# Optimization experiments

Hardware: AMD Instinct MI355X
Metric: run time of the kernel (lower is better)

Reference implementation:

```python
import jax, jax.numpy as jnp
import numpy as np

B, S, D_IN, D_H = 8, 4096, 256, 512
EPS = 1e-6


def setup_inputs() -> dict:
    key = jax.random.key(0)
    ks = jax.random.split(key, 5)
    scale = 1.0 / np.sqrt(D_IN)  # torch Linear default init scale (uniform bound)
    x = jax.random.normal(ks[0], (B, S, D_IN), dtype=jnp.float32)
    Wi = jax.random.normal(ks[1], (D_IN, D_H), dtype=jnp.float32) * scale
    Wf = jax.random.normal(ks[2], (D_IN, D_H), dtype=jnp.float32) * scale
    Wo = jax.random.normal(ks[3], (D_IN, D_H), dtype=jnp.float32) * scale
    Wz = jax.random.normal(ks[4], (D_IN, D_H), dtype=jnp.float32) * scale
    zb = jnp.zeros((D_H,), dtype=jnp.float32)
    return {"x": x, "Wi": Wi, "bi": zb, "Wf": Wf, "bf": zb,
            "Wo": Wo, "bo": zb, "Wz": Wz, "bz": zb}


def _xlstm_forward(x, Wi, bi, Wf, bf, Wo, bo, Wz, bz):
    # Batched projections over all timesteps at once: [B,S,D_H] each.
    i_t = jnp.exp(jnp.clip(jnp.einsum('bsd,dh->bsh', x, Wi) + bi, -20.0, 0.0))
    f_t = jnp.exp(jnp.clip(jnp.einsum('bsd,dh->bsh', x, Wf) + bf, -20.0, 0.0))
    o_t = jax.nn.sigmoid(jnp.einsum('bsd,dh->bsh', x, Wo) + bo)
    z_t = jnp.tanh(jnp.einsum('bsd,dh->bsh', x, Wz) + bz)

    def step(carry, gates):
        c, n = carry
        i, f, o, z = gates
        c = f * c + i * z
        n = f * n + i
        h = o * (c / (n + EPS))
        return (c, n), h

    c0 = jnp.zeros((x.shape[0], Wi.shape[1]), dtype=x.dtype)
    n0 = jnp.ones((x.shape[0], Wi.shape[1]), dtype=x.dtype)
    # time-major scan over the recurrence
    gates_tm = tuple(jnp.swapaxes(g, 0, 1) for g in (i_t, f_t, o_t, z_t))  # [S,B,H]
    _, h_tm = jax.lax.scan(step, (c0, n0), gates_tm)
    return jnp.swapaxes(h_tm, 0, 1)  # [B,S,H]


def reference(x, Wi, bi, Wf, bf, Wo, bo, Wz, bz):
    return _xlstm_forward(x, Wi, bi, Wf, bf, Wo, bo, Wz, bz)
```

## Files before the change

kernel.cpp:

```cpp
#include <hip/hip_runtime.h>
#include <hip/hip_bf16.h>
#include <cstdint>
#include <cstddef>

typedef __hip_bfloat16 bf16;
typedef __attribute__((ext_vector_type(8))) short short8;
typedef __attribute__((ext_vector_type(4))) short short4v;
typedef __attribute__((ext_vector_type(4))) float floatx4;

#define BB 8
#define SS 4096
#define DIN 256
#define DH 512
#define NCH 256
#define CHUNK 16

__device__ __forceinline__ float b2f(bf16 v) { return __bfloat162float(v); }
__device__ __forceinline__ float sh2f(short v) {
    unsigned int u = ((unsigned int)(unsigned short)v) << 16;
    float f; __builtin_memcpy(&f, &u, 4); return f;
}
__device__ __forceinline__ float frcp(float x) { return __builtin_amdgcn_rcpf(x); }
__device__ __forceinline__ short f2sh(float a) {
    bf16 bv = __float2bfloat16(a);
    short sv; __builtin_memcpy(&sv, &bv, 2); return sv;
}

__global__ __launch_bounds__(256) void convert_x(
    const float* __restrict__ X, bf16* __restrict__ Xb)
{
    const int idx = blockIdx.x * 256 + threadIdx.x;
    float4 v = ((const float4*)X)[idx];
    bf16 o[4] = {__float2bfloat16(v.x), __float2bfloat16(v.y),
                 __float2bfloat16(v.z), __float2bfloat16(v.w)};
    ((short4v*)Xb)[idx] = *(const short4v*)o;
}

__global__ __launch_bounds__(256) void transpose_w(
    const float* __restrict__ Wi, const float* __restrict__ Wf,
    const float* __restrict__ Wo, const float* __restrict__ Wz,
    bf16* __restrict__ Wt)
{
    int o = blockIdx.x * 256 + threadIdx.x;
    int r = o >> 8;
    int k = o & 255;
    int y = r >> 7;
    int c = r & 127;
    int g = c >> 5;
    int h = y * 32 + (c & 31);
    const float* W = (g == 0) ? Wi : (g == 1) ? Wf : (g == 2) ? Wo : Wz;
    Wt[o] = __float2bfloat16(W[(size_t)k * DH + h]);
}

__device__ __forceinline__ void load16_lds(const bf16* g, short* l)
{
    __builtin_amdgcn_global_load_lds(
        (const __attribute__((address_space(1))) unsigned int*)g,
        (__attribute__((address_space(3))) unsigned int*)l,
        16, 0, 0);
}

__global__ __launch_bounds__(256) void gemm_mfma(
    const bf16* __restrict__ Xb, const bf16* __restrict__ Wt,
    const float* __restrict__ bi, const float* __restrict__ bfv,
    const float* __restrict__ bo, const float* __restrict__ bz,
    bf16* __restrict__ Pi, bf16* __restrict__ Pf,
    bf16* __restrict__ Po, bf16* __restrict__ Pz,
    float* __restrict__ Aa, float* __restrict__ Bca, float* __restrict__ Bna,
    int nb)
{
    __shared__ __align__(16) short smem[3 * 8192];

    const int cpx = gridDim.x >> 3;
    const int logical = ((int)blockIdx.x & 7) * cpx + ((int)blockIdx.x >> 3);
    const int y  = logical & 15;
    const int m0 = (logical >> 4) * 128;
    const int n0 = y * 128;

    const int tid  = threadIdx.x;
    const int wave = tid >> 6, lane = tid & 63;
    const int wm   = (wave >> 1) * 64, wn = (wave & 1) * 64;
    const int l15  = lane & 15;
    const int q    = lane >> 4;

    floatx4 acc[4][4];
#pragma unroll
    for (int i = 0; i < 4; i++)
#pragma unroll
        for (int j = 0; j < 4; j++) acc[i][j] = (floatx4){0.f, 0.f, 0.f, 0.f};

    const int r_ld = tid >> 2;
    const int c_ld = tid & 3;
    const bf16* agp0 = Xb + (size_t)(m0 + r_ld) * DIN + c_ld * 8;
    const bf16* agp1 = Xb + (size_t)(m0 + 64 + r_ld) * DIN + c_ld * 8;
    const bf16* bgp0 = Wt + (size_t)(n0 + r_ld) * DIN + c_ld * 8;
    const bf16* bgp1 = Wt + (size_t)(n0 + 64 + r_ld) * DIN + c_ld * 8;

#define STAGE(K0, BUF)                                            \
    do {                                                          \
        short* A_ = smem + (BUF) * 8192;                          \
        short* B_ = A_ + 4096;                                    \
        load16_lds(agp0 + (K0), &A_[tid * 8]);                    \
        load16_lds(agp1 + (K0), &A_[2048 + tid * 8]);             \
        load16_lds(bgp0 + (K0), &B_[tid * 8]);                    \
        load16_lds(bgp1 + (K0), &B_[2048 + tid * 8]);             \
    } while (0)

    STAGE(0, 0);
    STAGE(32, 1);

#pragma unroll
    for (int k = 0; k < 8; k++) {
        if (k < 6) STAGE((k + 2) * 32, (k + 2) % 3);
        if (k < 6)       asm volatile("s_waitcnt vmcnt(8)" ::: "memory");
        else if (k == 6) asm volatile("s_waitcnt vmcnt(4)" ::: "memory");
        else             asm volatile("s_waitcnt vmcnt(0)" ::: "memory");
        __builtin_amdgcn_s_barrier();
        __builtin_amdgcn_sched_barrier(0);

        const short* A = smem + (k % 3) * 8192;
        const short* B = A + 4096;
        short8 af[4], bfr[4];
#pragma unroll
        for (int ti = 0; ti < 4; ti++)
            af[ti] = *(const short8*)&A[(wm + ti * 16 + l15) * 32 + q * 8];
#pragma unroll
        for (int tj = 0; tj < 4; tj++)
            bfr[tj] = *(const short8*)&B[(wn + tj * 16 + l15) * 32 + q * 8];
#pragma unroll
        for (int ti = 0; ti < 4; ti++)
#pragma unroll
            for (int tj = 0; tj < 4; tj++)
                acc[ti][tj] = __builtin_amdgcn_mfma_f32_16x16x32_bf16(
                    af[ti], bfr[tj], acc[ti][tj], 0, 0, 0);
        asm volatile("s_waitcnt lgkmcnt(0)" ::: "memory");
        __builtin_amdgcn_sched_barrier(0);
        __builtin_amdgcn_s_barrier();
    }
#undef STAGE

#pragma unroll
    for (int ti = 0; ti < 4; ti++) {
        const int mrow = wm + ti * 16 + q * 4;
#pragma unroll
        for (int tj = 0; tj < 4; tj++) {
            const int cb = wn + tj * 16;
            const int g  = cb >> 5;
            const int c  = cb + l15;
            const float* bp = (g == 0) ? bi : (g == 1) ? bfv
                            : (g == 2) ? bo : bz;
            const float bsv = bp[y * 32 + (c & 31)];
#pragma unroll
            for (int r = 0; r < 4; r++) {
                const float v = acc[ti][tj][r] + bsv;
                float a;
                if (g == 0 || g == 1) {
                    a = __expf(fminf(fmaxf(v, -20.f), 0.f));
                } else if (g == 2) {
                    a = frcp(1.f + __expf(-v));
                } else {
                    a = 1.f - 2.f * frcp(__expf(2.f * v) + 1.f);
                }
                smem[(mrow + r) * 132 + c] = f2sh(a);
            }
        }
    }
    __syncthreads();

    const int bidx = m0 / SS;

    {
        const int cp  = (tid & 31) * 4;
        const int g2  = cp >> 5;
        const int hb  = y * 32 + (cp & 31);
        bf16* pl = ((g2 == 0) ? Pi : (g2 == 1) ? Pf : (g2 == 2) ? Po : Pz) + hb;
        const int r0 = tid >> 5;
#pragma unroll
        for (int t = 0; t < 16; t++) {
            const int row = t * 8 + r0;
            short4v v = *(const short4v*)&smem[row * 132 + cp];
            *(short4v*)(pl + (size_t)(m0 + row) * DH) = v;
        }
    }

    {
        const int hh = tid & 31;
        const int ch = tid >> 5;
        float A = 1.f, Bc = 0.f, Bn = 0.f;
        const short* base = &smem[(ch * CHUNK) * 132];
#pragma unroll
        for (int s = 0; s < CHUNK; s++) {
            const short* rp = base + s * 132;
            const float iv = sh2f(rp[hh]);
            const float f  = sh2f(rp[32 + hh]);
            const float zv = sh2f(rp[96 + hh]);
            Bc = fmaf(f, Bc, iv * zv);
            Bn = fmaf(f, Bn, iv);
            A *= f;
        }
        const int ch_g = ((m0 % SS) >> 4) + ch;
        const int hgl  = y * 32 + hh;
        const size_t cidx = (size_t)(ch_g * nb + bidx) * DH + hgl;
        Aa[cidx] = A; Bca[cidx] = Bc; Bna[cidx] = Bn;
    }
}

__global__ __launch_bounds__(256) void scan_chunks(
    float* __restrict__ Aa, float* __restrict__ Bca,
    const float* __restrict__ Bna, int nb)
{
    __shared__ float sA[4][64], sBc[4][64], sBn[4][64];
    const int tid = threadIdx.x;
    const int t   = blockIdx.x * 64 + (tid & 63);
    const int s   = tid >> 6;
    const int stride = nb * DH;
    const int SEG = NCH / 4;

    float A = 1.f, Bc = 0.f, Bn = 0.f;
    for (int k = 0; k < SEG; k++) {
        const size_t cidx = (size_t)(s * SEG + k) * stride + t;
        const float a  = Aa[cidx];
        const float bc = Bca[cidx];
        const float bn = Bna[cidx];
        Bc = fmaf(a, Bc, bc);
        Bn = fmaf(a, Bn, bn);
        A *= a;
    }
    sA[s][tid & 63] = A; sBc[s][tid & 63] = Bc; sBn[s][tid & 63] = Bn;
    __syncthreads();

    float c = 0.f, n = 1.f;
#pragma unroll
    for (int s2 = 0; s2 < 3; s2++) {
        if (s2 < s) {
            const float a  = sA[s2][tid & 63];
            const float nc = fmaf(a, c, sBc[s2][tid & 63]);
            n = fmaf(a, n, sBn[s2][tid & 63]);
            c = nc;
        }
    }

    for (int k = 0; k < SEG; k++) {
        const size_t cidx = (size_t)(s * SEG + k) * stride + t;
        const float a  = Aa[cidx];
        const float bc = Bca[cidx];
        const float bn = Bna[cidx];
        Aa[cidx] = c; Bca[cidx] = n;
        const float nc = fmaf(a, c, bc);
        n = fmaf(a, n, bn);
        c = nc;
    }
}

__global__ __launch_bounds__(256) void scan_emit(
    const bf16* __restrict__ Pi, const bf16* __restrict__ Pf,
    const bf16* __restrict__ Po, const bf16* __restrict__ Pz,
    const float* __restrict__ Cs, const float* __restrict__ Ns,
    float* __restrict__ out, int nb)
{
    const int tid = threadIdx.x;
    const int ch  = blockIdx.x * 2 + (tid >> 7);
    const int b   = blockIdx.y;
    const int hg  = (tid & 127) * 4;
    const size_t base = ((size_t)(b * SS + ch * CHUNK)) * DH + hg;
    const size_t cidx = (size_t)(ch * nb + b) * DH + hg;

    float c[4], n[4];
    *(floatx4*)c = *(const floatx4*)(Cs + cidx);
    *(floatx4*)n = *(const floatx4*)(Ns + cidx);

#pragma unroll 4
    for (int s = 0; s < CHUNK; s++) {
        const size_t o = base + (size_t)s * DH;
        short4v i4 = *(const short4v*)(Pi + o);
        short4v f4 = *(const short4v*)(Pf + o);
        short4v o4 = *(const short4v*)(Po + o);
        short4v z4 = *(const short4v*)(Pz + o);
        float h[4];
#pragma unroll
        for (int j = 0; j < 4; j++) {
            const float f  = sh2f(f4[j]);
            const float iv = sh2f(i4[j]);
            const float ov = sh2f(o4[j]);
            const float zv = sh2f(z4[j]);
            c[j] = fmaf(f, c[j], iv * zv);
            n[j] = fmaf(f, n[j], iv);
            h[j] = ov * c[j] * frcp(n[j] + 1e-6f);
        }
        *(floatx4*)(out + o) = *(floatx4*)h;
    }
}

extern "C" void kernel_launch(void* const* d_in, const int* in_sizes, int n_in,
                              void* d_out, int out_size, void* d_ws, size_t ws_size,
                              hipStream_t stream)
{
    const float* x   = (const float*)d_in[0];
    const float* Wi  = (const float*)d_in[1];
    const float* bi  = (const float*)d_in[2];
    const float* Wf  = (const float*)d_in[3];
    const float* bfv = (const float*)d_in[4];
    const float* Wo  = (const float*)d_in[5];
    const float* bo  = (const float*)d_in[6];
    const float* Wz  = (const float*)d_in[7];
    const float* bz  = (const float*)d_in[8];
    float* out = (float*)d_out;

    int nb = BB;
    while (nb > 1) {
        size_t need = (1u << 20)
                    + (size_t)nb * SS * DIN * 2
                    + 4 * (size_t)nb * SS * DH * 2
                    + 3 * (size_t)NCH * nb * DH * 4;
        if (need <= ws_size) break;
        nb >>= 1;
    }

    const size_t plane = (size_t)nb * SS * DH;
    bf16* Wt = (bf16*)d_ws;
    bf16* Xb = (bf16*)((char*)d_ws + (1u << 20));
    bf16* Pi = Xb + (size_t)nb * SS * DIN;
    bf16* Pf = Pi + plane;
    bf16* Po = Pf + plane;
    bf16* Pz = Po + plane;
    float* Aa  = (float*)(Pz + plane);
    float* Bca = Aa  + (size_t)NCH * nb * DH;
    float* Bna = Bca + (size_t)NCH * nb * DH;

    transpose_w<<<2048, 256, 0, stream>>>(Wi, Wf, Wo, Wz, Wt);

    for (int b0 = 0; b0 < BB; b0 += nb) {
        const float* Xsrc = x   + (size_t)b0 * SS * DIN;
        float*       Ob   = out + (size_t)b0 * SS * DH;
        convert_x<<<nb * 1024, 256, 0, stream>>>(Xsrc, Xb);
        gemm_mfma<<<nb * 512, 256, 0, stream>>>(
            Xb, Wt, bi, bfv, bo, bz, Pi, Pf, Po, Pz, Aa, Bca, Bna, nb);
        scan_chunks<<<nb * 8, 256, 0, stream>>>(Aa, Bca, Bna, nb);
        scan_emit<<<dim3(NCH / 2, nb), 256, 0, stream>>>(
            Pi, Pf, Po, Pz, Aa, Bca, Ob, nb);
    }
}
```

Before: 233.2 us.

## Recompute gate GEMM in emit pass instead of storing bf16 gate planes

Drops the four bf16 gate planes written by the GEMM and read back by scan_emit. The GEMM is now a template that runs twice: the first pass produces only per-chunk scan summaries, and the second pass recomputes the gates and emits h directly from the chunk carries. This trades roughly 64 MB of intermediate traffic for a second GEMM. It also shrinks shared memory and swaps the 3-stage load pipeline for a simpler 2-stage loop that waits on vmcnt(0) every iteration, which may expose more load latency.

```diff
diff --git a/kernel.cpp b/kernel.cpp
--- a/kernel.cpp
+++ b/kernel.cpp
@@ -15,7 +15,6 @@
 #define NCH 256
 #define CHUNK 16
 
-__device__ __forceinline__ float b2f(bf16 v) { return __bfloat162float(v); }
 __device__ __forceinline__ float sh2f(short v) {
     unsigned int u = ((unsigned int)(unsigned short)v) << 16;
     float f; __builtin_memcpy(&f, &u, 4); return f;
@@ -60,16 +59,15 @@
         16, 0, 0);
 }
 
-__global__ __launch_bounds__(256) void gemm_mfma(
+template<int MODE>
+__global__ __launch_bounds__(256) void gemm_fused(
     const bf16* __restrict__ Xb, const bf16* __restrict__ Wt,
     const float* __restrict__ bi, const float* __restrict__ bfv,
     const float* __restrict__ bo, const float* __restrict__ bz,
-    bf16* __restrict__ Pi, bf16* __restrict__ Pf,
-    bf16* __restrict__ Po, bf16* __restrict__ Pz,
     float* __restrict__ Aa, float* __restrict__ Bca, float* __restrict__ Bna,
-    int nb)
-{
-    __shared__ __align__(16) short smem[3 * 8192];
+    float* __restrict__ out, int nb)
+{
+    __shared__ __align__(16) short smem[128 * 132];
 
     const int cpx = gridDim.x >> 3;
     const int logical = ((int)blockIdx.x & 7) * cpx + ((int)blockIdx.x >> 3);
@@ -107,18 +105,14 @@
     } while (0)
 
     STAGE(0, 0);
-    STAGE(32, 1);
+    asm volatile("s_waitcnt vmcnt(0)" ::: "memory");
+    __builtin_amdgcn_s_barrier();
 
 #pragma unroll
     for (int k = 0; k < 8; k++) {
-        if (k < 6) STAGE((k + 2) * 32, (k + 2) % 3);
-        if (k < 6)       asm volatile("s_waitcnt vmcnt(8)" ::: "memory");
-        else if (k == 6) asm volatile("s_waitcnt vmcnt(4)" ::: "memory");
-        else             asm volatile("s_waitcnt vmcnt(0)" ::: "memory");
-        __builtin_amdgcn_s_barrier();
-        __builtin_amdgcn_sched_barrier(0);
-
-        const short* A = smem + (k % 3) * 8192;
+        const int cur = k & 1;
+        if (k < 7) STAGE((k + 1) * 32, cur ^ 1);
+        const short* A = smem + cur * 8192;
         const short* B = A + 4096;
         short8 af[4], bfr[4];
 #pragma unroll
@@ -133,8 +127,7 @@
             for (int tj = 0; tj < 4; tj++)
                 acc[ti][tj] = __builtin_amdgcn_mfma_f32_16x16x32_bf16(
                     af[ti], bfr[tj], acc[ti][tj], 0, 0, 0);
-        asm volatile("s_waitcnt lgkmcnt(0)" ::: "memory");
-        __builtin_amdgcn_sched_barrier(0);
+        asm volatile("s_waitcnt vmcnt(0) lgkmcnt(0)" ::: "memory");
         __builtin_amdgcn_s_barrier();
     }
 #undef STAGE
@@ -146,6 +139,7 @@
         for (int tj = 0; tj < 4; tj++) {
             const int cb = wn + tj * 16;
             const int g  = cb >> 5;
+            if (MODE == 0 && g == 2) continue;
             const int c  = cb + l15;
             const float* bp = (g == 0) ? bi : (g == 1) ? bfv
                             : (g == 2) ? bo : bz;
@@ -168,26 +162,14 @@
     __syncthreads();
 
     const int bidx = m0 / SS;
-
-    {
-        const int cp  = (tid & 31) * 4;
-        const int g2  = cp >> 5;
-        const int hb  = y * 32 + (cp & 31);
-        bf16* pl = ((g2 == 0) ? Pi : (g2 == 1) ? Pf : (g2 == 2) ? Po : Pz) + hb;
-        const int r0 = tid >> 5;
-#pragma unroll
-        for (int t = 0; t < 16; t++) {
-            const int row = t * 8 + r0;
-            short4v v = *(const short4v*)&smem[row * 132 + cp];
-            *(short4v*)(pl + (size_t)(m0 + row) * DH) = v;
-        }
-    }
-
-    {
-        const int hh = tid & 31;
-        const int ch = tid >> 5;
+    const int hh   = tid & 31;
+    const int ch   = tid >> 5;
+    const int ch_g = ((m0 % SS) >> 4) + ch;
+    const size_t cidx = (size_t)(ch_g * nb + bidx) * DH + y * 32 + hh;
+    const short* base = &smem[(ch * CHUNK) * 132];
+
+    if (MODE == 0) {
         float A = 1.f, Bc = 0.f, Bn = 0.f;
-        const short* base = &smem[(ch * CHUNK) * 132];
 #pragma unroll
         for (int s = 0; s < CHUNK; s++) {
             const short* rp = base + s * 132;
@@ -198,10 +180,22 @@
             Bn = fmaf(f, Bn, iv);
             A *= f;
         }
-        const int ch_g = ((m0 % SS) >> 4) + ch;
-        const int hgl  = y * 32 + hh;
-        const size_t cidx = (size_t)(ch_g * nb + bidx) * DH + hgl;
         Aa[cidx] = A; Bca[cidx] = Bc; Bna[cidx] = Bn;
+    } else {
+        float c = Aa[cidx];
+        float n = Bca[cidx];
+        float* orow = out + (size_t)(m0 + ch * CHUNK) * DH + y * 32 + hh;
+#pragma unroll
+        for (int s = 0; s < CHUNK; s++) {
+            const short* rp = base + s * 132;
+            const float iv = sh2f(rp[hh]);
+            const float f  = sh2f(rp[32 + hh]);
+            const float ov = sh2f(rp[64 + hh]);
+            const float zv = sh2f(rp[96 + hh]);
+            c = fmaf(f, c, iv * zv);
+            n = fmaf(f, n, iv);
+            orow[(size_t)s * DH] = ov * c * frcp(n + 1e-6f);
+        }
     }
 }
 
@@ -249,45 +243,6 @@
         const float nc = fmaf(a, c, bc);
         n = fmaf(a, n, bn);
         c = nc;
-    }
-}
-
-__global__ __launch_bounds__(256) void scan_emit(
-    const bf16* __restrict__ Pi, const bf16* __restrict__ Pf,
-    const bf16* __restrict__ Po, const bf16* __restrict__ Pz,
-    const float* __restrict__ Cs, const float* __restrict__ Ns,
-    float* __restrict__ out, int nb)
-{
-    const int tid = threadIdx.x;
-    const int ch  = blockIdx.x * 2 + (tid >> 7);
-    const int b   = blockIdx.y;
-    const int hg  = (tid & 127) * 4;
-    const size_t base = ((size_t)(b * SS + ch * CHUNK)) * DH + hg;
-    const size_t cidx = (size_t)(ch * nb + b) * DH + hg;
-
-    float c[4], n[4];
-    *(floatx4*)c = *(const floatx4*)(Cs + cidx);
-    *(floatx4*)n = *(const floatx4*)(Ns + cidx);
-
-#pragma unroll 4
-    for (int s = 0; s < CHUNK; s++) {
-        const size_t o = base + (size_t)s * DH;
-        short4v i4 = *(const short4v*)(Pi + o);
-        short4v f4 = *(const short4v*)(Pf + o);
-        short4v o4 = *(const short4v*)(Po + o);
-        short4v z4 = *(const short4v*)(Pz + o);
-        float h[4];
-#pragma unroll
-        for (int j = 0; j < 4; j++) {
-            const float f  = sh2f(f4[j]);
-            const float iv = sh2f(i4[j]);
-            const float ov = sh2f(o4[j]);
-            const float zv = sh2f(z4[j]);
-            c[j] = fmaf(f, c[j], iv * zv);
-            n[j] = fmaf(f, n[j], iv);
-            h[j] = ov * c[j] * frcp(n[j] + 1e-6f);
-        }
-        *(floatx4*)(out + o) = *(floatx4*)h;
     }
 }
 
@@ -310,20 +265,14 @@
     while (nb > 1) {
         size_t need = (1u << 20)
                     + (size_t)nb * SS * DIN * 2
-                    + 4 * (size_t)nb * SS * DH * 2
                     + 3 * (size_t)NCH * nb * DH * 4;
         if (need <= ws_size) break;
         nb >>= 1;
     }
 
-    const size_t plane = (size_t)nb * SS * DH;
     bf16* Wt = (bf16*)d_ws;
     bf16* Xb = (bf16*)((char*)d_ws + (1u << 20));
-    bf16* Pi = Xb + (size_t)nb * SS * DIN;
-    bf16* Pf = Pi + plane;
-    bf16* Po = Pf + plane;
-    bf16* Pz = Po + plane;
-    float* Aa  = (float*)(Pz + plane);
+    float* Aa  = (float*)(Xb + (size_t)nb * SS * DIN);
     float* Bca = Aa  + (size_t)NCH * nb * DH;
     float* Bna = Bca + (size_t)NCH * nb * DH;
 
@@ -333,10 +282,10 @@
         const float* Xsrc = x   + (size_t)b0 * SS * DIN;
         float*       Ob   = out + (size_t)b0 * SS * DH;
         convert_x<<<nb * 1024, 256, 0, stream>>>(Xsrc, Xb);
-        gemm_mfma<<<nb * 512, 256, 0, stream>>>(
-            Xb, Wt, bi, bfv, bo, bz, Pi, Pf, Po, Pz, Aa, Bca, Bna, nb);
+        gemm_fused<0><<<nb * 512, 256, 0, stream>>>(
+            Xb, Wt, bi, bfv, bo, bz, Aa, Bca, Bna, nullptr, nb);
         scan_chunks<<<nb * 8, 256, 0, stream>>>(Aa, Bca, Bna, nb);
-        scan_emit<<<dim3(NCH / 2, nb), 256, 0, stream>>>(
-            Pi, Pf, Po, Pz, Aa, Bca, Ob, nb);
-    }
-}
+        gemm_fused<1><<<nb * 512, 256, 0, stream>>>(
+            Xb, Wt, bi, bfv, bo, bz, Aa, Bca, Bna, Ob, nb);
+    }
+}
```

Result: slower. 241.8 us (+3.7%).

## Merge weight transpose and x conversion into one prep kernel; double-buffer GEMM

Applied to the files above, without the earlier changes.

Combines the weight transpose/bf16 cast and the x-to-bf16 conversion into a single prep launch, which saves one kernel launch per call. The GEMM goes from a three-stage to a two-stage LDS pipeline and drops the sched_barrier hints. The LDS array is resized to 128*132 shorts, which still covers the two 8192-short buffers and leaves room that the unseen epilogue may use for staging. Less prefetch depth may expose more global-load latency, but the lower LDS use could allow more resident blocks.

```diff
diff --git a/kernel.cpp b/kernel.cpp
--- a/kernel.cpp
+++ b/kernel.cpp
@@ -15,7 +15,6 @@
 #define NCH 256
 #define CHUNK 16
 
-__device__ __forceinline__ float b2f(bf16 v) { return __bfloat162float(v); }
 __device__ __forceinline__ float sh2f(short v) {
     unsigned int u = ((unsigned int)(unsigned short)v) << 16;
     float f; __builtin_memcpy(&f, &u, 4); return f;
@@ -26,30 +25,31 @@
     short sv; __builtin_memcpy(&sv, &bv, 2); return sv;
 }
 
-__global__ __launch_bounds__(256) void convert_x(
-    const float* __restrict__ X, bf16* __restrict__ Xb)
-{
-    const int idx = blockIdx.x * 256 + threadIdx.x;
-    float4 v = ((const float4*)X)[idx];
-    bf16 o[4] = {__float2bfloat16(v.x), __float2bfloat16(v.y),
-                 __float2bfloat16(v.z), __float2bfloat16(v.w)};
-    ((short4v*)Xb)[idx] = *(const short4v*)o;
-}
-
-__global__ __launch_bounds__(256) void transpose_w(
+__global__ __launch_bounds__(256) void prep(
     const float* __restrict__ Wi, const float* __restrict__ Wf,
     const float* __restrict__ Wo, const float* __restrict__ Wz,
-    bf16* __restrict__ Wt)
-{
-    int o = blockIdx.x * 256 + threadIdx.x;
-    int r = o >> 8;
-    int k = o & 255;
-    int y = r >> 7;
-    int c = r & 127;
-    int g = c >> 5;
-    int h = y * 32 + (c & 31);
-    const float* W = (g == 0) ? Wi : (g == 1) ? Wf : (g == 2) ? Wo : Wz;
-    Wt[o] = __float2bfloat16(W[(size_t)k * DH + h]);
+    bf16* __restrict__ Wt,
+    const float* __restrict__ X, bf16* __restrict__ Xb, int tblk)
+{
+    const int bx = blockIdx.x;
+    const int tid = threadIdx.x;
+    if (bx < tblk) {
+        int o = bx * 256 + tid;
+        int r = o >> 8;
+        int k = o & 255;
+        int y = r >> 7;
+        int c = r & 127;
+        int g = c >> 5;
+        int h = y * 32 + (c & 31);
+        const float* W = (g == 0) ? Wi : (g == 1) ? Wf : (g == 2) ? Wo : Wz;
+        Wt[o] = __float2bfloat16(W[(size_t)k * DH + h]);
+    } else {
+        const int idx = (bx - tblk) * 256 + tid;
+        float4 v = ((const float4*)X)[idx];
+        bf16 o4[4] = {__float2bfloat16(v.x), __float2bfloat16(v.y),
+                      __float2bfloat16(v.z), __float2bfloat16(v.w)};
+        ((short4v*)Xb)[idx] = *(const short4v*)o4;
+    }
 }
 
 __device__ __forceinline__ void load16_lds(const bf16* g, short* l)
@@ -69,7 +69,7 @@
     float* __restrict__ Aa, float* __restrict__ Bca, float* __restrict__ Bna,
     int nb)
 {
-    __shared__ __align__(16) short smem[3 * 8192];
+    __shared__ __align__(16) short smem[128 * 132];
 
     const int cpx = gridDim.x >> 3;
     const int logical = ((int)blockIdx.x & 7) * cpx + ((int)blockIdx.x >> 3);
@@ -107,18 +107,16 @@
     } while (0)
 
     STAGE(0, 0);
-    STAGE(32, 1);
 
 #pragma unroll
     for (int k = 0; k < 8; k++) {
-        if (k < 6) STAGE((k + 2) * 32, (k + 2) % 3);
-        if (k < 6)       asm volatile("s_waitcnt vmcnt(8)" ::: "memory");
-        else if (k == 6) asm volatile("s_waitcnt vmcnt(4)" ::: "memory");
-        else             asm volatile("s_waitcnt vmcnt(0)" ::: "memory");
+        const int cur = k & 1;
+        if (k < 7) STAGE((k + 1) * 32, cur ^ 1);
+        if (k < 7) asm volatile("s_waitcnt vmcnt(4)" ::: "memory");
+        else       asm volatile("s_waitcnt vmcnt(0)" ::: "memory");
         __builtin_amdgcn_s_barrier();
-        __builtin_amdgcn_sched_barrier(0);
-
-        const short* A = smem + (k % 3) * 8192;
+
+        const short* A = smem + cur * 8192;
         const short* B = A + 4096;
         short8 af[4], bfr[4];
 #pragma unroll
@@ -134,7 +132,6 @@
                 acc[ti][tj] = __builtin_amdgcn_mfma_f32_16x16x32_bf16(
                     af[ti], bfr[tj], acc[ti][tj], 0, 0, 0);
         asm volatile("s_waitcnt lgkmcnt(0)" ::: "memory");
-        __builtin_amdgcn_sched_barrier(0);
         __builtin_amdgcn_s_barrier();
     }
 #undef STAGE
@@ -327,12 +324,12 @@
     float* Bca = Aa  + (size_t)NCH * nb * DH;
     float* Bna = Bca + (size_t)NCH * nb * DH;
 
-    transpose_w<<<2048, 256, 0, stream>>>(Wi, Wf, Wo, Wz, Wt);
-
     for (int b0 = 0; b0 < BB; b0 += nb) {
         const float* Xsrc = x   + (size_t)b0 * SS * DIN;
         float*       Ob   = out + (size_t)b0 * SS * DH;
-        convert_x<<<nb * 1024, 256, 0, stream>>>(Xsrc, Xb);
+        const int tblk = (b0 == 0) ? 2048 : 0;
+        prep<<<tblk + nb * 1024, 256, 0, stream>>>(
+            Wi, Wf, Wo, Wz, Wt, Xsrc, Xb, tblk);
         gemm_mfma<<<nb * 512, 256, 0, stream>>>(
             Xb, Wt, bi, bfv, bo, bz, Pi, Pf, Po, Pz, Aa, Bca, Bna, nb);
         scan_chunks<<<nb * 8, 256, 0, stream>>>(Aa, Bca, Bna, nb);
```

Measured after the change: 228.4 us. -2.1%, faster.
